# Kernel tuning notes

Hardware: AMD Instinct MI355X
Metric: run time of the kernel (lower is better)

Reference implementation:

```python
import jax, jax.numpy as jnp
import numpy as np

B, N, C = 1, 768, 384
H, P = 12, 4
DP = 128  # dim_pair
HP3 = H * P * 3  # 144


def linear(x, W, b):
    # torch nn.Linear: y = x @ W.T + b, W shape (out, in)
    return jnp.einsum('...i,oi->...o', x, W) + b


def setup_inputs() -> dict:
    key = jax.random.key(0)
    ks = jax.random.split(key, 24)
    w = lambda k, *s: jax.random.normal(k, s, jnp.float32) * 0.02
    inp = {
        'single': jax.random.normal(ks[0], (B, N, C), jnp.float32),
        'pair': jax.random.normal(ks[1], (B, N, N, DP), jnp.float32),
        'rot': jax.random.normal(ks[2], (B, N, 3, 3), jnp.float32),
        'trans': jax.random.normal(ks[3], (B, N, 3), jnp.float32),
        'Wq': w(ks[4], C, C), 'bq': jnp.zeros((C,), jnp.float32),
        'Wk': w(ks[5], C, C), 'bk': jnp.zeros((C,), jnp.float32),
        'Wv': w(ks[6], C, C), 'bv': jnp.zeros((C,), jnp.float32),
        'Wpb': w(ks[7], H, DP), 'bpb': jnp.zeros((H,), jnp.float32),
        'Wqp': w(ks[8], HP3, C), 'bqp': jnp.zeros((HP3,), jnp.float32),
        'Wkp': w(ks[9], HP3, C), 'bkp': jnp.zeros((HP3,), jnp.float32),
        'Wvp': w(ks[10], HP3, C), 'bvp': jnp.zeros((HP3,), jnp.float32),
        'Wo': w(ks[11], C, C), 'bo': jnp.zeros((C,), jnp.float32),
        'Wpo': w(ks[12], C, HP3), 'bpo': jnp.zeros((C,), jnp.float32),
        'ln_w': jnp.ones((C,), jnp.float32), 'ln_b': jnp.zeros((C,), jnp.float32),
    }
    return inp


def reference(single, pair, rot, trans, Wq, bq, Wk, bk, Wv, bv, Wpb, bpb,
              Wqp, bqp, Wkp, bkp, Wvp, bvp, Wo, bo, Wpo, bpo, ln_w, ln_b):
    Ch = C // H
    scale = Ch ** -0.5
    q = linear(single, Wq, bq).reshape(B, N, H, Ch)
    k = linear(single, Wk, bk).reshape(B, N, H, Ch)
    v = linear(single, Wv, bv).reshape(B, N, H, Ch)
    pair_bias = jnp.transpose(linear(pair, Wpb, bpb), (0, 3, 1, 2))  # (B,H,N,N)

    q_pts = linear(single, Wqp, bqp).reshape(B, N, H, P, 3)
    k_pts = linear(single, Wkp, bkp).reshape(B, N, H, P, 3)
    v_pts = linear(single, Wvp, bvp).reshape(B, N, H, P, 3)
    t = trans[:, :, None, None, :]  # (B,N,1,1,3)
    # rotate local points into global frame: p @ R + t
    q_g = jnp.einsum('bnhpd,bnde->bnhpe', q_pts, rot) + t
    k_g = jnp.einsum('bnhpd,bnde->bnhpe', k_pts, rot) + t
    v_g = jnp.einsum('bnhpd,bnde->bnhpe', v_pts, rot) + t

    q2 = jnp.sum(q_g ** 2, axis=(3, 4))  # (B,N,H)
    k2 = jnp.sum(k_g ** 2, axis=(3, 4))
    qk = jnp.einsum('bnhpd,bmhpd->bhnm', q_g, k_g)
    q2h = jnp.transpose(q2, (0, 2, 1))  # (B,H,N)
    k2h = jnp.transpose(k2, (0, 2, 1))
    point_logits = -0.5 * (q2h[..., :, None] + k2h[..., None, :] - 2.0 * qk) * scale
    scalar_logits = jnp.einsum('bnhc,bmhc->bhnm', q, k) * scale
    attn = jax.nn.softmax(scalar_logits + pair_bias + point_logits, axis=-1)

    weighted_scalar = jnp.einsum('bhnm,bmhc->bnhc', attn, v).reshape(B, N, C)
    weighted_points = jnp.einsum('bhnm,bmhpd->bnhpd', attn, v_g).reshape(B, N, HP3)
    point_proj = linear(weighted_points, Wpo, bpo)
    out = linear(weighted_scalar + point_proj, Wo, bo)

    x = single + out
    mu = jnp.mean(x, axis=-1, keepdims=True)
    var = jnp.mean((x - mu) ** 2, axis=-1, keepdims=True)
    return (x - mu) / jnp.sqrt(var + 1e-5) * ln_w + ln_b
```

## Files before the change

### kernel.cpp

```cpp
#include <hip/hip_runtime.h>
#include <math.h>

#define NRES 768
#define CDIM 384
#define HEADS 12
#define SCALE 0.17677669529663687f

typedef _Float16 f16;
typedef _Float16 __attribute__((ext_vector_type(8))) f16x8;
typedef float __attribute__((ext_vector_type(4))) f32x4;

__device__ __forceinline__ f16x8 ldcvt8(const float* __restrict__ p) {
  float4 a = *(const float4*)p;
  float4 b = *(const float4*)(p + 4);
  f16x8 r = {(f16)a.x, (f16)a.y, (f16)a.z, (f16)a.w,
             (f16)b.x, (f16)b.y, (f16)b.z, (f16)b.w};
  return r;
}

__device__ __forceinline__ void mfma_step(f16 (*As)[64], f16 (*Bs)[64],
                                          int w, int lg, int lr, f32x4* acc) {
#pragma unroll
  for (int ks = 0; ks < 2; ++ks) {
    f16x8 af = *(const f16x8*)&As[w * 16 + lr][((ks * 4 + lg) ^ (lr & 7)) * 8];
#pragma unroll
    for (int c = 0; c < 4; ++c) {
      f16x8 bf = *(const f16x8*)&Bs[c * 16 + lr][((ks * 4 + lg) ^ (lr & 7)) * 8];
      acc[c] = __builtin_amdgcn_mfma_f32_16x16x32_f16(af, bf, acc[c], 0, 0, 0);
    }
  }
}

__global__ __launch_bounds__(256) void mega_gemm(
    const float* __restrict__ single,
    const float* __restrict__ Wq, const float* __restrict__ Wk, const float* __restrict__ Wv,
    const float* __restrict__ Wqp, const float* __restrict__ Wkp, const float* __restrict__ Wvp,
    const float* __restrict__ bq, const float* __restrict__ bk, const float* __restrict__ bv,
    const float* __restrict__ bqp, const float* __restrict__ bkp, const float* __restrict__ bvp,
    const float* __restrict__ Wpo, const float* __restrict__ bpo, const float* __restrict__ Wo,
    f16* __restrict__ Wcomb, f16* __restrict__ S16) {
  __shared__ f16 As[64][64];
  __shared__ f16 Bs[64][64];
  const int bx = blockIdx.x, by = blockIdx.y;
  const int t = threadIdx.x;
  const int w = t >> 6, l = t & 63;
  const int lg = l >> 4, lr = l & 15;
  const f16 z0 = (f16)0.f;
  f32x4 acc[4] = {{0.f,0.f,0.f,0.f},{0.f,0.f,0.f,0.f},{0.f,0.f,0.f,0.f},{0.f,0.f,0.f,0.f}};

  if (bx < 25) {
    const int bm = by * 64, bn = bx * 64;
    for (int k0 = 0; k0 < 384; k0 += 64) {
      __syncthreads();
#pragma unroll
      for (int cc = 0; cc < 2; ++cc) {
        int c = t + cc * 256;
        int row = c >> 3, k8 = c & 7;
        int sw = (k8 ^ (row & 7)) * 8;
        *(f16x8*)&As[row][sw] = ldcvt8(single + (size_t)(bm + row) * 384 + k0 + k8 * 8);
        int o = bn + row;
        const float* bsrc;
        if (o < 384)       bsrc = Wq  + (size_t)o * 384;
        else if (o < 768)  bsrc = Wk  + (size_t)(o - 384) * 384;
        else if (o < 1152) bsrc = Wv  + (size_t)(o - 768) * 384;
        else if (o < 1296) bsrc = Wqp + (size_t)(o - 1152) * 384;
        else if (o < 1440) bsrc = Wkp + (size_t)(o - 1296) * 384;
        else if (o < 1584) bsrc = Wvp + (size_t)(o - 1440) * 384;
        else               bsrc = nullptr;
        f16x8 vb8 = {z0, z0, z0, z0, z0, z0, z0, z0};
        if (bsrc) vb8 = ldcvt8(bsrc + k0 + k8 * 8);
        *(f16x8*)&Bs[row][sw] = vb8;
      }
      __syncthreads();
      mfma_step(As, Bs, w, lg, lr, acc);
    }
#pragma unroll
    for (int c = 0; c < 4; ++c) {
      int col = bn + c * 16 + lr;
      if (col >= 1584) continue;
      float bb;
      if (col < 384)       bb = bq[col];
      else if (col < 768)  bb = bk[col - 384];
      else if (col < 1152) bb = bv[col - 768];
      else if (col < 1296) bb = bqp[col - 1152];
      else if (col < 1440) bb = bkp[col - 1296];
      else                 bb = bvp[col - 1440];
#pragma unroll
      for (int r = 0; r < 4; ++r) {
        int row = bm + w * 16 + lg * 4 + r;
        S16[(size_t)row * 1584 + col] = (f16)(acc[c][r] + bb);
      }
    }
  } else if (by < 6) {
    const int bm = by * 64, bn = (bx - 25) * 64;
    for (int k0 = 0; k0 < 384; k0 += 64) {
      __syncthreads();
#pragma unroll
      for (int cc = 0; cc < 2; ++cc) {
        int c = t + cc * 256;
        int row = c >> 3, k8 = c & 7;
        int sw = (k8 ^ (row & 7)) * 8;
        *(f16x8*)&As[row][sw] = ldcvt8(Wo + (size_t)(bm + row) * 384 + k0 + k8 * 8);
        int pr = bn + row;
        f16x8 vb8 = {z0, z0, z0, z0, z0, z0, z0, z0};
        if (pr < 144) {
#pragma unroll
          for (int j = 0; j < 8; ++j) vb8[j] = (f16)Wpo[(size_t)(k0 + k8 * 8 + j) * 144 + pr];
        } else if (pr == 144) {
#pragma unroll
          for (int j = 0; j < 8; ++j) vb8[j] = (f16)bpo[k0 + k8 * 8 + j];
        }
        *(f16x8*)&Bs[row][sw] = vb8;
      }
      __syncthreads();
      mfma_step(As, Bs, w, lg, lr, acc);
    }
#pragma unroll
    for (int c = 0; c < 4; ++c) {
      int col = bn + c * 16 + lr;
      if (col >= 192) continue;
#pragma unroll
      for (int r = 0; r < 4; ++r)
        Wcomb[(size_t)(bm + w * 16 + lg * 4 + r) * 192 + col] = (f16)acc[c][r];
    }
  }
}

__global__ __launch_bounds__(256) void final_gemm(
    const f16* __restrict__ attn_cat, const float* __restrict__ Wo,
    const f16* __restrict__ Wcomb, const float* __restrict__ bo,
    const float* __restrict__ single, float* __restrict__ xb) {
  __shared__ f16 As[64][64];
  __shared__ f16 Bs[64][64];
  const int t = threadIdx.x;
  const int w = t >> 6, l = t & 63;
  const int lg = l >> 4, lr = l & 15;
  const int bm = blockIdx.y * 64, bn = blockIdx.x * 64;
  f32x4 acc[4] = {{0.f,0.f,0.f,0.f},{0.f,0.f,0.f,0.f},{0.f,0.f,0.f,0.f},{0.f,0.f,0.f,0.f}};
  for (int k0 = 0; k0 < 576; k0 += 64) {
    __syncthreads();
#pragma unroll
    for (int cc = 0; cc < 2; ++cc) {
      int c = t + cc * 256;
      int row = c >> 3, k8 = c & 7;
      int sw = (k8 ^ (row & 7)) * 8;
      *(f16x8*)&As[row][sw] = *(const f16x8*)(attn_cat + (size_t)(bm + row) * 576 + k0 + k8 * 8);
      f16x8 vb8;
      if (k0 < 384) vb8 = ldcvt8(Wo + (size_t)(bn + row) * 384 + k0 + k8 * 8);
      else          vb8 = *(const f16x8*)(Wcomb + (size_t)(bn + row) * 192 + (k0 - 384) + k8 * 8);
      *(f16x8*)&Bs[row][sw] = vb8;
    }
    __syncthreads();
    mfma_step(As, Bs, w, lg, lr, acc);
  }
#pragma unroll
  for (int c = 0; c < 4; ++c) {
    int col = bn + c * 16 + lr;
    float bb = bo[col];
#pragma unroll
    for (int r = 0; r < 4; ++r) {
      int row = bm + w * 16 + lg * 4 + r;
      xb[(size_t)row * 384 + col] = acc[c][r] + bb + single[(size_t)row * 384 + col];
    }
  }
}

__global__ __launch_bounds__(64) void rot_feats3(
    const f16* __restrict__ S16, const float* __restrict__ rot, const float* __restrict__ trans,
    f16* __restrict__ qf, f16* __restrict__ kf, f16* __restrict__ vfT) {
  const int n = blockIdx.x * 64 + threadIdx.x;
  const int h = blockIdx.y;
  const f16* Sr = S16 + (size_t)n * 1584;
  float R[9], T[3];
#pragma unroll
  for (int i = 0; i < 9; ++i) R[i] = rot[n * 9 + i];
#pragma unroll
  for (int i = 0; i < 3; ++i) T[i] = trans[n * 3 + i];
  f16 qh[64], kh[64];
  f16x8 qv4[4], kv4[4], vv4[4];
#pragma unroll
  for (int j = 0; j < 4; ++j) {
    qv4[j] = *(const f16x8*)(Sr + h * 32 + j * 8);
    kv4[j] = *(const f16x8*)(Sr + 384 + h * 32 + j * 8);
    vv4[j] = *(const f16x8*)(Sr + 768 + h * 32 + j * 8);
  }
#pragma unroll
  for (int c = 0; c < 32; ++c) {
    qh[c] = (f16)(SCALE * (float)qv4[c >> 3][c & 7]);
    vfT[((size_t)(h * 48 + c)) * NRES + n] = vv4[c >> 3][c & 7];
  }
#pragma unroll
  for (int j = 0; j < 4; ++j) *(f16x8*)&kh[j * 8] = kv4[j];
  float qp[12], kp[12], vp[12];
#pragma unroll
  for (int e = 0; e < 12; ++e) {
    qp[e] = (float)Sr[1152 + h * 12 + e];
    kp[e] = (float)Sr[1296 + h * 12 + e];
    vp[e] = (float)Sr[1440 + h * 12 + e];
  }
  float q2 = 0.f, k2 = 0.f;
#pragma unroll
  for (int p = 0; p < 4; ++p) {
#pragma unroll
    for (int e = 0; e < 3; ++e) {
      float qg = qp[p*3+0] * R[e] + qp[p*3+1] * R[3+e] + qp[p*3+2] * R[6+e] + T[e];
      float kg = kp[p*3+0] * R[e] + kp[p*3+1] * R[3+e] + kp[p*3+2] * R[6+e] + T[e];
      float vg = vp[p*3+0] * R[e] + vp[p*3+1] * R[3+e] + vp[p*3+2] * R[6+e] + T[e];
      qh[32 + p*3 + e] = (f16)(SCALE * qg); q2 += qg * qg;
      kh[32 + p*3 + e] = (f16)kg;           k2 += kg * kg;
      vfT[((size_t)(h * 48 + 32 + p*3 + e)) * NRES + n] = (f16)vg;
    }
  }
  qh[44] = (f16)(-0.5f * SCALE * q2); qh[45] = (f16)1.f;
  kh[44] = (f16)1.f;                  kh[45] = (f16)(-0.5f * SCALE * k2);
#pragma unroll
  for (int c = 46; c < 64; ++c) { qh[c] = (f16)0.f; kh[c] = (f16)0.f; }
#pragma unroll
  for (int c = 44; c < 48; ++c) vfT[((size_t)(h * 48 + c)) * NRES + n] = (f16)0.f;
  f16* qo = qf + ((size_t)(h * NRES + n)) * 64;
  f16* ko = kf + ((size_t)(h * NRES + n)) * 64;
#pragma unroll
  for (int j = 0; j < 8; ++j) {
    *(f16x8*)&qo[j * 8] = *(const f16x8*)&qh[j * 8];
    *(f16x8*)&ko[j * 8] = *(const f16x8*)&kh[j * 8];
  }
}

__global__ __launch_bounds__(512) void fused_attn(
    const float* __restrict__ pair, const float* __restrict__ Wpb, const float* __restrict__ bpb,
    const f16* __restrict__ qf, const f16* __restrict__ kf, const f16* __restrict__ vfT,
    f16* __restrict__ partNh, float* __restrict__ partD) {
  __shared__ f16 bias_l[12 * 1160];
  const int t = threadIdx.x;
  const int w = t >> 6, l = t & 63;
  const int lg = l >> 4, lr = l & 15;
  const int mblk = blockIdx.x;
  const int q0 = blockIdx.y * 16;
  const int m0 = mblk * 64;

  f16x8 bfr[4];
#pragma unroll
  for (int ks = 0; ks < 4; ++ks)
#pragma unroll
    for (int j = 0; j < 8; ++j)
      bfr[ks][j] = (f16)((lr < HEADS) ? Wpb[lr * 128 + ks * 32 + lg * 8 + j] : 0.f);
  const float bh = (lr < HEADS) ? bpb[lr] : 0.f;

#pragma unroll
  for (int g8 = 0; g8 < 8; ++g8) {
    const int g = w * 8 + g8;
    const int rowf = g * 16 + lr;
    const int nf = rowf >> 6, mf = rowf & 63;
    const float* ap = pair + (((size_t)(q0 + nf)) * NRES + (m0 + mf)) * 128 + lg * 8;
    f32x4 acc = {0.f, 0.f, 0.f, 0.f};
#pragma unroll
    for (int ks = 0; ks < 4; ++ks) {
      float4 a0 = *(const float4*)(ap + ks * 32);
      float4 a1 = *(const float4*)(ap + ks * 32 + 4);
      f16x8 af = {(f16)a0.x, (f16)a0.y, (f16)a0.z, (f16)a0.w,
                  (f16)a1.x, (f16)a1.y, (f16)a1.z, (f16)a1.w};
      acc = __builtin_amdgcn_mfma_f32_16x16x32_f16(af, bfr[ks], acc, 0, 0, 0);
    }
    if (lr < HEADS) {
#pragma unroll
      for (int r = 0; r < 4; ++r) {
        int rowo = g * 16 + lg * 4 + r;
        bias_l[lr * 1160 + (rowo >> 6) * 72 + (rowo & 63)] = (f16)(acc[r] + bh);
      }
    }
  }
  __syncthreads();

  for (int h = w; h < 12; h += 8) {
    const f16* qrow = qf + ((size_t)(h * NRES + q0 + lr)) * 64;
    f16x8 qa0 = *(const f16x8*)(qrow + lg * 8);
    f16x8 qa1 = *(const f16x8*)(qrow + 32 + lg * 8);
    float den[4] = {0.f, 0.f, 0.f, 0.f};
#pragma unroll
    for (int mc = 0; mc < 4; ++mc) {
      const f16* krow = kf + ((size_t)(h * NRES + m0 + mc * 16 + lr)) * 64;
      f16x8 kb0 = *(const f16x8*)(krow + lg * 8);
      f16x8 kb1 = *(const f16x8*)(krow + 32 + lg * 8);
      f32x4 s = {0.f, 0.f, 0.f, 0.f};
      s = __builtin_amdgcn_mfma_f32_16x16x32_f16(qa0, kb0, s, 0, 0, 0);
      s = __builtin_amdgcn_mfma_f32_16x16x32_f16(qa1, kb1, s, 0, 0, 0);
#pragma unroll
      for (int r = 0; r < 4; ++r) {
        const int pidx = h * 1160 + (lg * 4 + r) * 72 + mc * 16 + lr;
        float b = (float)bias_l[pidx];
        float e = __expf(s[r] + b);
        den[r] += e;
        bias_l[pidx] = (f16)e;
      }
    }
#pragma unroll
    for (int r = 0; r < 4; ++r) {
      float d = den[r];
      d += __shfl_xor(d, 1); d += __shfl_xor(d, 2);
      d += __shfl_xor(d, 4); d += __shfl_xor(d, 8);
      if (lr == 0)
        partD[((size_t)mblk * NRES + q0 + lg * 4 + r) * 12 + h] = d;
    }
#pragma unroll
    for (int c3 = 0; c3 < 3; ++c3) {
      f32x4 a = {0.f, 0.f, 0.f, 0.f};
#pragma unroll
      for (int ks = 0; ks < 2; ++ks) {
        f16x8 pa = *(const f16x8*)&bias_l[h * 1160 + lr * 72 + ks * 32 + lg * 8];
        f16x8 vb = *(const f16x8*)(vfT + ((size_t)(h * 48 + c3 * 16 + lr)) * NRES + m0 + ks * 32 + lg * 8);
        a = __builtin_amdgcn_mfma_f32_16x16x32_f16(pa, vb, a, 0, 0, 0);
      }
#pragma unroll
      for (int r = 0; r < 4; ++r)
        partNh[((size_t)mblk * NRES + q0 + lg * 4 + r) * 576 + h * 48 + c3 * 16 + lr] = (f16)a[r];
    }
  }
}

__global__ __launch_bounds__(576) void attn_reduce(
    const f16* __restrict__ partNh, const float* __restrict__ partD,
    f16* __restrict__ attn_cat) {
  const int n = blockIdx.x;
  const int hc = threadIdx.x;
  const int h = hc / 48, c = hc - h * 48;
  float num = 0.f, den = 0.f;
#pragma unroll
  for (int mc = 0; mc < 12; ++mc) {
    num += (float)partNh[((size_t)mc * NRES + n) * 576 + hc];
    den += partD[((size_t)mc * NRES + n) * 12 + h];
  }
  float val = num / den;
  if (c < 32)      attn_cat[(size_t)n * 576 + h * 32 + c] = (f16)val;
  else if (c < 44) attn_cat[(size_t)n * 576 + 384 + h * 12 + (c - 32)] = (f16)val;
  if (hc < 48)     attn_cat[(size_t)n * 576 + 528 + hc] = (f16)(hc == 0 ? 1.f : 0.f);
}

__global__ __launch_bounds__(64) void ln_kernel(
    const float* __restrict__ x, const float* __restrict__ w, const float* __restrict__ b,
    float* __restrict__ out) {
  int n = blockIdx.x;
  int l = threadIdx.x;
  const float* xr = x + (size_t)n * CDIM;
  float v[6];
  float s = 0.f;
#pragma unroll
  for (int i = 0; i < 6; ++i) { v[i] = xr[l + 64 * i]; s += v[i]; }
#pragma unroll
  for (int o = 32; o; o >>= 1) s += __shfl_xor(s, o);
  float mu = s * (1.f / 384.f);
  float vs = 0.f;
#pragma unroll
  for (int i = 0; i < 6; ++i) { float d = v[i] - mu; vs += d * d; }
#pragma unroll
  for (int o = 32; o; o >>= 1) vs += __shfl_xor(vs, o);
  float rstd = rsqrtf(vs * (1.f / 384.f) + 1e-5f);
  float* orow = out + (size_t)n * CDIM;
#pragma unroll
  for (int i = 0; i < 6; ++i) {
    int c = l + 64 * i;
    orow[c] = (v[i] - mu) * rstd * w[c] + b[c];
  }
}

extern "C" void kernel_launch(void* const* d_in, const int* in_sizes, int n_in,
                              void* d_out, int out_size, void* d_ws, size_t ws_size,
                              hipStream_t stream) {
  const float* single = (const float*)d_in[0];
  const float* pair   = (const float*)d_in[1];
  const float* rot    = (const float*)d_in[2];
  const float* trans  = (const float*)d_in[3];
  const float* Wq  = (const float*)d_in[4];
  const float* bq  = (const float*)d_in[5];
  const float* Wk  = (const float*)d_in[6];
  const float* bk  = (const float*)d_in[7];
  const float* Wv  = (const float*)d_in[8];
  const float* bv  = (const float*)d_in[9];
  const float* Wpb = (const float*)d_in[10];
  const float* bpb = (const float*)d_in[11];
  const float* Wqp = (const float*)d_in[12];
  const float* bqp = (const float*)d_in[13];
  const float* Wkp = (const float*)d_in[14];
  const float* bkp = (const float*)d_in[15];
  const float* Wvp = (const float*)d_in[16];
  const float* bvp = (const float*)d_in[17];
  const float* Wo  = (const float*)d_in[18];
  const float* bo  = (const float*)d_in[19];
  const float* Wpo = (const float*)d_in[20];
  const float* bpo = (const float*)d_in[21];
  const float* lnw = (const float*)d_in[22];
  const float* lnb = (const float*)d_in[23];

  float* ws = (float*)d_ws;
  f16* S16      = (f16*)ws; ws += 768 * 1584 / 2;
  f16* Wcomb    = (f16*)ws; ws += 384 * 192 / 2;
  f16* qf       = (f16*)ws; ws += 12 * 768 * 64 / 2;
  f16* kf       = (f16*)ws; ws += 12 * 768 * 64 / 2;
  f16* vfT      = (f16*)ws; ws += 12 * 48 * 768 / 2;
  f16* partNh   = (f16*)ws; ws += 12 * 768 * 576 / 2;
  float* partD  = ws;       ws += 12 * 768 * 12;
  f16* attn_cat = (f16*)ws; ws += 768 * 576 / 2;
  float* xb     = ws;       ws += 768 * 384;

  mega_gemm<<<dim3(28, 12), 256, 0, stream>>>(single,
                                              Wq, Wk, Wv, Wqp, Wkp, Wvp,
                                              bq, bk, bv, bqp, bkp, bvp,
                                              Wpo, bpo, Wo, Wcomb, S16);
  rot_feats3<<<dim3(12, 12), 64, 0, stream>>>(S16, rot, trans, qf, kf, vfT);
  fused_attn<<<dim3(12, 48), 512, 0, stream>>>(pair, Wpb, bpb, qf, kf, vfT, partNh, partD);
  attn_reduce<<<768, 576, 0, stream>>>(partNh, partD, attn_cat);
  final_gemm<<<dim3(6, 12), 256, 0, stream>>>(attn_cat, Wo, Wcomb, bo, single, xb);
  ln_kernel<<<768, 64, 0, stream>>>(xb, lnw, lnb, (float*)d_out);
}
```

Measured before the change: 130.0 us.

## Move pair-bias projection into first kernel to overlap with QKV GEMMs

The pair-bias projection (the pass that streams the large pair tensor) moves out of the attention kernel and into the first launch, where it runs alongside the QKV/point and Wo·Wpo GEMM tiles. The goal is to hide that bandwidth-heavy pass behind the GEMM work and make the attention kernel lighter. The GEMM blocks also change from 256 to 512 threads, with each wave now computing two 16-column tiles. The cost is an extra fp16 bias buffer of 12×768×768 that is written to global memory and read back, which adds memory traffic.

```diff
diff --git a/kernel.cpp b/kernel.cpp
--- a/kernel.cpp
+++ b/kernel.cpp
@@ -31,31 +31,80 @@
   }
 }
 
-__global__ __launch_bounds__(256) void mega_gemm(
+__global__ __launch_bounds__(512) void k1_mega(
+    const float* __restrict__ pair, const float* __restrict__ Wpb, const float* __restrict__ bpb,
     const float* __restrict__ single,
     const float* __restrict__ Wq, const float* __restrict__ Wk, const float* __restrict__ Wv,
     const float* __restrict__ Wqp, const float* __restrict__ Wkp, const float* __restrict__ Wvp,
     const float* __restrict__ bq, const float* __restrict__ bk, const float* __restrict__ bv,
     const float* __restrict__ bqp, const float* __restrict__ bkp, const float* __restrict__ bvp,
     const float* __restrict__ Wpo, const float* __restrict__ bpo, const float* __restrict__ Wo,
-    f16* __restrict__ Wcomb, f16* __restrict__ S16) {
-  __shared__ f16 As[64][64];
-  __shared__ f16 Bs[64][64];
-  const int bx = blockIdx.x, by = blockIdx.y;
+    f16* __restrict__ biasb, f16* __restrict__ Wcomb, f16* __restrict__ S16) {
+  __shared__ f16 smem[12 * 1160];
+  const int bid = blockIdx.x;
   const int t = threadIdx.x;
   const int w = t >> 6, l = t & 63;
   const int lg = l >> 4, lr = l & 15;
   const f16 z0 = (f16)0.f;
-  f32x4 acc[4] = {{0.f,0.f,0.f,0.f},{0.f,0.f,0.f,0.f},{0.f,0.f,0.f,0.f},{0.f,0.f,0.f,0.f}};
-
-  if (bx < 25) {
-    const int bm = by * 64, bn = bx * 64;
+
+  if (bid < 576) {
+    f16* bias_l = smem;
+    const int mblk = bid % 12;
+    const int q0 = (bid / 12) * 16;
+    const int m0 = mblk * 64;
+    f16x8 bfr[4];
+#pragma unroll
+    for (int ks = 0; ks < 4; ++ks)
+#pragma unroll
+      for (int j = 0; j < 8; ++j)
+        bfr[ks][j] = (f16)((lr < HEADS) ? Wpb[lr * 128 + ks * 32 + lg * 8 + j] : 0.f);
+    const float bh = (lr < HEADS) ? bpb[lr] : 0.f;
+#pragma unroll
+    for (int g8 = 0; g8 < 8; ++g8) {
+      const int g = w * 8 + g8;
+      const int rowf = g * 16 + lr;
+      const int nf = rowf >> 6, mf = rowf & 63;
+      const float* ap = pair + (((size_t)(q0 + nf)) * NRES + (m0 + mf)) * 128 + lg * 8;
+      f32x4 acc = {0.f, 0.f, 0.f, 0.f};
+#pragma unroll
+      for (int ks = 0; ks < 4; ++ks) {
+        float4 a0 = *(const float4*)(ap + ks * 32);
+        float4 a1 = *(const float4*)(ap + ks * 32 + 4);
+        f16x8 af = {(f16)a0.x, (f16)a0.y, (f16)a0.z, (f16)a0.w,
+                    (f16)a1.x, (f16)a1.y, (f16)a1.z, (f16)a1.w};
+        acc = __builtin_amdgcn_mfma_f32_16x16x32_f16(af, bfr[ks], acc, 0, 0, 0);
+      }
+      if (lr < HEADS) {
+#pragma unroll
+        for (int r = 0; r < 4; ++r) {
+          int rowo = g * 16 + lg * 4 + r;
+          bias_l[lr * 1160 + (rowo >> 6) * 72 + (rowo & 63)] = (f16)(acc[r] + bh);
+        }
+      }
+    }
+    __syncthreads();
+    for (int i = t; i < 12 * 16 * 8; i += 512) {
+      int h = i >> 7;
+      int rem = i & 127;
+      int row = rem >> 3, c8 = rem & 7;
+      *(f16x8*)(biasb + (size_t)h * (NRES * NRES) + (size_t)(q0 + row) * NRES + m0 + c8 * 8) =
+          *(const f16x8*)&bias_l[h * 1160 + row * 72 + c8 * 8];
+    }
+    return;
+  }
+
+  f16 (*As)[64] = (f16(*)[64])smem;
+  f16 (*Bs)[64] = (f16(*)[64])(smem + 4096);
+  const int wm = w & 3, wn = w >> 2;
+  f32x4 acc[2] = {{0.f,0.f,0.f,0.f},{0.f,0.f,0.f,0.f}};
+
+  if (bid < 876) {
+    const int i = bid - 576;
+    const int bm = (i / 25) * 64, bn = (i % 25) * 64;
     for (int k0 = 0; k0 < 384; k0 += 64) {
       __syncthreads();
-#pragma unroll
-      for (int cc = 0; cc < 2; ++cc) {
-        int c = t + cc * 256;
-        int row = c >> 3, k8 = c & 7;
+      {
+        int row = t >> 3, k8 = t & 7;
         int sw = (k8 ^ (row & 7)) * 8;
         *(f16x8*)&As[row][sw] = ldcvt8(single + (size_t)(bm + row) * 384 + k0 + k8 * 8);
         int o = bn + row;
@@ -72,11 +121,19 @@
         *(f16x8*)&Bs[row][sw] = vb8;
       }
       __syncthreads();
-      mfma_step(As, Bs, w, lg, lr, acc);
-    }
-#pragma unroll
-    for (int c = 0; c < 4; ++c) {
-      int col = bn + c * 16 + lr;
+#pragma unroll
+      for (int ks = 0; ks < 2; ++ks) {
+        f16x8 af = *(const f16x8*)&As[wm * 16 + lr][((ks * 4 + lg) ^ (lr & 7)) * 8];
+#pragma unroll
+        for (int j = 0; j < 2; ++j) {
+          f16x8 bf = *(const f16x8*)&Bs[(wn * 2 + j) * 16 + lr][((ks * 4 + lg) ^ (lr & 7)) * 8];
+          acc[j] = __builtin_amdgcn_mfma_f32_16x16x32_f16(af, bf, acc[j], 0, 0, 0);
+        }
+      }
+    }
+#pragma unroll
+    for (int j = 0; j < 2; ++j) {
+      int col = bn + (wn * 2 + j) * 16 + lr;
       if (col >= 1584) continue;
       float bb;
       if (col < 384)       bb = bq[col];
@@ -87,18 +144,17 @@
       else                 bb = bvp[col - 1440];
 #pragma unroll
       for (int r = 0; r < 4; ++r) {
-        int row = bm + w * 16 + lg * 4 + r;
-        S16[(size_t)row * 1584 + col] = (f16)(acc[c][r] + bb);
-      }
-    }
-  } else if (by < 6) {
-    const int bm = by * 64, bn = (bx - 25) * 64;
+        int row = bm + wm * 16 + lg * 4 + r;
+        S16[(size_t)row * 1584 + col] = (f16)(acc[j][r] + bb);
+      }
+    }
+  } else {
+    const int i = bid - 876;
+    const int bm = (i / 3) * 64, bn = (i % 3) * 64;
     for (int k0 = 0; k0 < 384; k0 += 64) {
       __syncthreads();
-#pragma unroll
-      for (int cc = 0; cc < 2; ++cc) {
-        int c = t + cc * 256;
-        int row = c >> 3, k8 = c & 7;
+      {
+        int row = t >> 3, k8 = t & 7;
         int sw = (k8 ^ (row & 7)) * 8;
         *(f16x8*)&As[row][sw] = ldcvt8(Wo + (size_t)(bm + row) * 384 + k0 + k8 * 8);
         int pr = bn + row;
@@ -113,15 +169,23 @@
         *(f16x8*)&Bs[row][sw] = vb8;
       }
       __syncthreads();
-      mfma_step(As, Bs, w, lg, lr, acc);
-    }
-#pragma unroll
-    for (int c = 0; c < 4; ++c) {
-      int col = bn + c * 16 + lr;
+#pragma unroll
+      for (int ks = 0; ks < 2; ++ks) {
+        f16x8 af = *(const f16x8*)&As[wm * 16 + lr][((ks * 4 + lg) ^ (lr & 7)) * 8];
+#pragma unroll
+        for (int j = 0; j < 2; ++j) {
+          f16x8 bf = *(const f16x8*)&Bs[(wn * 2 + j) * 16 + lr][((ks * 4 + lg) ^ (lr & 7)) * 8];
+          acc[j] = __builtin_amdgcn_mfma_f32_16x16x32_f16(af, bf, acc[j], 0, 0, 0);
+        }
+      }
+    }
+#pragma unroll
+    for (int j = 0; j < 2; ++j) {
+      int col = bn + (wn * 2 + j) * 16 + lr;
       if (col >= 192) continue;
 #pragma unroll
       for (int r = 0; r < 4; ++r)
-        Wcomb[(size_t)(bm + w * 16 + lg * 4 + r) * 192 + col] = (f16)acc[c][r];
+        Wcomb[(size_t)(bm + wm * 16 + lg * 4 + r) * 192 + col] = (f16)acc[j][r];
     }
   }
 }
@@ -226,8 +290,8 @@
   }
 }
 
-__global__ __launch_bounds__(512) void fused_attn(
-    const float* __restrict__ pair, const float* __restrict__ Wpb, const float* __restrict__ bpb,
+__global__ __launch_bounds__(512) void attn_k3(
+    const f16* __restrict__ biasb,
     const f16* __restrict__ qf, const f16* __restrict__ kf, const f16* __restrict__ vfT,
     f16* __restrict__ partNh, float* __restrict__ partD) {
   __shared__ f16 bias_l[12 * 1160];
@@ -238,36 +302,12 @@
   const int q0 = blockIdx.y * 16;
   const int m0 = mblk * 64;
 
-  f16x8 bfr[4];
-#pragma unroll
-  for (int ks = 0; ks < 4; ++ks)
-#pragma unroll
-    for (int j = 0; j < 8; ++j)
-      bfr[ks][j] = (f16)((lr < HEADS) ? Wpb[lr * 128 + ks * 32 + lg * 8 + j] : 0.f);
-  const float bh = (lr < HEADS) ? bpb[lr] : 0.f;
-
-#pragma unroll
-  for (int g8 = 0; g8 < 8; ++g8) {
-    const int g = w * 8 + g8;
-    const int rowf = g * 16 + lr;
-    const int nf = rowf >> 6, mf = rowf & 63;
-    const float* ap = pair + (((size_t)(q0 + nf)) * NRES + (m0 + mf)) * 128 + lg * 8;
-    f32x4 acc = {0.f, 0.f, 0.f, 0.f};
-#pragma unroll
-    for (int ks = 0; ks < 4; ++ks) {
-      float4 a0 = *(const float4*)(ap + ks * 32);
-      float4 a1 = *(const float4*)(ap + ks * 32 + 4);
-      f16x8 af = {(f16)a0.x, (f16)a0.y, (f16)a0.z, (f16)a0.w,
-                  (f16)a1.x, (f16)a1.y, (f16)a1.z, (f16)a1.w};
-      acc = __builtin_amdgcn_mfma_f32_16x16x32_f16(af, bfr[ks], acc, 0, 0, 0);
-    }
-    if (lr < HEADS) {
-#pragma unroll
-      for (int r = 0; r < 4; ++r) {
-        int rowo = g * 16 + lg * 4 + r;
-        bias_l[lr * 1160 + (rowo >> 6) * 72 + (rowo & 63)] = (f16)(acc[r] + bh);
-      }
-    }
+  for (int i = t; i < 12 * 16 * 8; i += 512) {
+    int h = i >> 7;
+    int rem = i & 127;
+    int row = rem >> 3, c8 = rem & 7;
+    *(f16x8*)&bias_l[h * 1160 + row * 72 + c8 * 8] =
+        *(const f16x8*)(biasb + (size_t)h * (NRES * NRES) + (size_t)(q0 + row) * NRES + m0 + c8 * 8);
   }
   __syncthreads();
 
@@ -393,6 +433,7 @@
   float* ws = (float*)d_ws;
   f16* S16      = (f16*)ws; ws += 768 * 1584 / 2;
   f16* Wcomb    = (f16*)ws; ws += 384 * 192 / 2;
+  f16* biasb    = (f16*)ws; ws += 12 * 768 * 768 / 2;
   f16* qf       = (f16*)ws; ws += 12 * 768 * 64 / 2;
   f16* kf       = (f16*)ws; ws += 12 * 768 * 64 / 2;
   f16* vfT      = (f16*)ws; ws += 12 * 48 * 768 / 2;
@@ -401,12 +442,12 @@
   f16* attn_cat = (f16*)ws; ws += 768 * 576 / 2;
   float* xb     = ws;       ws += 768 * 384;
 
-  mega_gemm<<<dim3(28, 12), 256, 0, stream>>>(single,
-                                              Wq, Wk, Wv, Wqp, Wkp, Wvp,
-                                              bq, bk, bv, bqp, bkp, bvp,
-                                              Wpo, bpo, Wo, Wcomb, S16);
+  k1_mega<<<894, 512, 0, stream>>>(pair, Wpb, bpb, single,
+                                   Wq, Wk, Wv, Wqp, Wkp, Wvp,
+                                   bq, bk, bv, bqp, bkp, bvp,
+                                   Wpo, bpo, Wo, biasb, Wcomb, S16);
   rot_feats3<<<dim3(12, 12), 64, 0, stream>>>(S16, rot, trans, qf, kf, vfT);
-  fused_attn<<<dim3(12, 48), 512, 0, stream>>>(pair, Wpb, bpb, qf, kf, vfT, partNh, partD);
+  attn_k3<<<dim3(12, 48), 512, 0, stream>>>(biasb, qf, kf, vfT, partNh, partD);
   attn_reduce<<<768, 576, 0, stream>>>(partNh, partD, attn_cat);
   final_gemm<<<dim3(6, 12), 256, 0, stream>>>(attn_cat, Wo, Wcomb, bo, single, xb);
   ln_kernel<<<768, 64, 0, stream>>>(xb, lnw, lnb, (float*)d_out);
```

Result: faster. 123.3 us (-5.2%).
